# Optimization experiments

Hardware: AMD Instinct MI355X
Metric: run time of the kernel (lower is better)

The kernel has to match this reference:

```python
import jax, jax.numpy as jnp
import numpy as np

N, E, D, L = 100000, 400000, 300, 5
BN_EPS = 1e-5


def setup_inputs() -> dict:
    key = jax.random.key(0)
    ks = jax.random.split(key, 8)
    x = jax.random.randint(ks[0], (N, 7), 0, 5)
    edge_index = jax.random.randint(ks[1], (2, E), 0, N)
    edge_attr = jax.random.randint(ks[2], (E, 4), 0, 2)
    s = 0.1
    atom_tables = jax.random.normal(ks[3], (7, 119, D), jnp.float32) * s
    bond_tables = jax.random.normal(ks[4], (L, 4, 6, D), jnp.float32) * s
    mlp_w1 = jax.random.normal(ks[5], (L, D, 2 * D), jnp.float32) * (1.0 / np.sqrt(D))
    mlp_b1 = jnp.zeros((L, 2 * D), jnp.float32)
    mlp_w2 = jax.random.normal(ks[6], (L, 2 * D, D), jnp.float32) * (1.0 / np.sqrt(2 * D))
    mlp_b2 = jnp.zeros((L, D), jnp.float32)
    bn_gamma = jnp.ones((L, D), jnp.float32)
    bn_beta = jnp.zeros((L, D), jnp.float32)
    return dict(x=x, edge_index=edge_index, edge_attr=edge_attr,
                atom_tables=atom_tables, bond_tables=bond_tables,
                mlp_w1=mlp_w1, mlp_b1=mlp_b1, mlp_w2=mlp_w2, mlp_b2=mlp_b2,
                bn_gamma=bn_gamma, bn_beta=bn_beta)


def reference(x, edge_index, edge_attr, atom_tables, bond_tables,
              mlp_w1, mlp_b1, mlp_w2, mlp_b2, bn_gamma, bn_beta):
    n = x.shape[0]
    # add self loops (PyG add_self_loops appends them)
    loop = jnp.arange(n)
    src = jnp.concatenate([edge_index[0], loop])  # message source j
    dst = jnp.concatenate([edge_index[1], loop])  # aggregation target i
    self_loop_attr = jnp.zeros((n, 4), edge_attr.dtype).at[:, 0].set(4)
    ea = jnp.concatenate([edge_attr, self_loop_attr], axis=0)  # [E+N, 4]

    # AtomEncoder: sum of 7 per-feature embeddings -> [N, D]
    h = atom_tables[jnp.arange(7), x].sum(axis=1)

    for l in range(L):
        # BondEncoder: sum of 4 per-feature embeddings -> [E+N, D]
        e_emb = bond_tables[l][jnp.arange(4), ea].sum(axis=1)
        # GIN message = x_j + edge_emb, aggr='add' by target node
        msg = h[src] + e_emb
        agg = jax.ops.segment_sum(msg, dst, num_segments=n)
        # GIN update MLP: Linear -> ReLU -> Linear
        hid = jax.nn.relu(agg @ mlp_w1[l] + mlp_b1[l])
        out = hid @ mlp_w2[l] + mlp_b2[l]
        # BatchNorm1d (training mode: batch stats, biased var)
        mu = out.mean(axis=0)
        var = out.var(axis=0)
        out = (out - mu) / jnp.sqrt(var + BN_EPS) * bn_gamma[l] + bn_beta[l]
        # drop_ratio = 0.0 -> dropout is identity; ReLU except last layer
        if l < L - 1:
            out = jax.nn.relu(out)
        h = out
    return h  # JK='last'
```

## Files before the change

### kernel.cpp

```cpp
#include <hip/hip_runtime.h>

typedef unsigned short u16;
typedef unsigned int   u32;
typedef __bf16 bf16x8 __attribute__((ext_vector_type(8)));
typedef float  f32x4  __attribute__((ext_vector_type(4)));

__device__ __forceinline__ u16 f2bf(float f) {
    u32 u = __builtin_bit_cast(u32, f);
    u = u + 0x7fffu + ((u >> 16) & 1u);
    return (u16)(u >> 16);
}
__device__ __forceinline__ float bflo(u32 u) { return __builtin_bit_cast(float, u << 16); }
__device__ __forceinline__ float bfhi(u32 u) { return __builtin_bit_cast(float, u & 0xffff0000u); }
__device__ __forceinline__ u32 pack2(float x, float y) { return (u32)f2bf(x) | ((u32)f2bf(y) << 16); }

#define NN 100000
#define EE 400000
#define DP 320
#define HP 640

__global__ void count_deg(const int* __restrict__ ei, int* __restrict__ deg, int E) {
    int e = blockIdx.x * 256 + threadIdx.x;
    if (e < E) atomicAdd(&deg[ei[E + e]], 1);
}

__global__ void scan1(const int* __restrict__ deg, int* __restrict__ out, int* __restrict__ bsums, int n) {
    __shared__ int lds[1024];
    int t = threadIdx.x;
    int i = blockIdx.x * 1024 + t;
    int v = (i < n) ? deg[i] : 0;
    lds[t] = v;
    __syncthreads();
    for (int d = 1; d < 1024; d <<= 1) {
        int add = (t >= d) ? lds[t - d] : 0;
        __syncthreads();
        lds[t] += add;
        __syncthreads();
    }
    if (i < n) out[i] = lds[t] - v;
    if (t == 1023) bsums[blockIdx.x] = lds[t];
}

__global__ void scan2(int* __restrict__ bsums, int nb) {
    __shared__ int lds[128];
    int t = threadIdx.x;
    int v = (t < nb) ? bsums[t] : 0;
    lds[t] = v;
    __syncthreads();
    for (int d = 1; d < 128; d <<= 1) {
        int add = (t >= d) ? lds[t - d] : 0;
        __syncthreads();
        lds[t] += add;
        __syncthreads();
    }
    if (t < nb) bsums[t] = lds[t] - v;
}

__global__ void scan3(int* __restrict__ out, const int* __restrict__ bsums, int n, int etot) {
    int i = blockIdx.x * 1024 + threadIdx.x;
    if (i < n) out[i] += bsums[blockIdx.x];
    else if (i == n) out[i] = etot;
}

__global__ void fill_csr(const int* __restrict__ ei, const int* __restrict__ ea,
                         int* __restrict__ cursors, u32* __restrict__ vals, int E) {
    int e = blockIdx.x * 256 + threadIdx.x;
    if (e >= E) return;
    int dst = ei[E + e];
    int src = ei[e];
    u32 code = (u32)((ea[e*4] & 1) | ((ea[e*4+1] & 1) << 1) | ((ea[e*4+2] & 1) << 2) | ((ea[e*4+3] & 1) << 3));
    int pos = atomicAdd(&cursors[dst], 1);
    vals[pos] = ((u32)src << 4) | code;
}

__global__ void conv_w1(const float* __restrict__ w, u16* __restrict__ wt) {
    int id = blockIdx.x * 256 + threadIdx.x;
    if (id >= 5 * HP * DP) return;
    int l = id / (HP * DP);
    int rem = id - l * (HP * DP);
    int n = rem / DP;
    int k = rem - n * DP;
    u16 v = 0;
    if (n < 600 && k < 300) v = f2bf(w[((size_t)l * 300 + k) * 600 + n]);
    wt[id] = v;
}
__global__ void conv_w2(const float* __restrict__ w, u16* __restrict__ wt) {
    int id = blockIdx.x * 256 + threadIdx.x;
    if (id >= 5 * DP * HP) return;
    int l = id / (DP * HP);
    int rem = id - l * (DP * HP);
    int n = rem / HP;
    int k = rem - n * HP;
    u16 v = 0;
    if (n < 300 && k < 600) v = f2bf(w[((size_t)l * 600 + k) * 300 + n]);
    wt[id] = v;
}

__global__ void atom_enc(const int* __restrict__ x, const float* __restrict__ at, u16* __restrict__ y) {
    const int i = blockIdx.x;
    const int d = threadIdx.x;
    __shared__ int xi[7];
    if (d < 7) xi[d] = x[i * 7 + d];
    __syncthreads();
    u16 v = 0;
    if (d < 300) {
        float s = 0.f;
        #pragma unroll
        for (int f = 0; f < 7; ++f) s += at[(f * 119 + xi[f]) * 300 + d];
        v = f2bf(s);
    }
    y[(size_t)i * DP + d] = v;
}

__global__ void bond_enc(const float* __restrict__ bt, float* __restrict__ emb) {
    const int c = blockIdx.x;
    const int d = threadIdx.x;
    float s = 0.f;
    if (d < 300) {
        if (c < 16) {
            #pragma unroll
            for (int f = 0; f < 4; ++f) s += bt[(f * 6 + ((c >> f) & 1)) * 300 + d];
        } else {
            s = bt[4 * 300 + d];
            #pragma unroll
            for (int f = 1; f < 4; ++f) s += bt[f * 6 * 300 + d];
        }
    }
    emb[c * DP + d] = s;
}

__global__ void bn_ss(const float* __restrict__ stats, const float* __restrict__ gamma,
                      const float* __restrict__ beta, float* __restrict__ scale,
                      float* __restrict__ shift, int n) {
    int d = threadIdx.x;
    float sc = 0.f, sh = 0.f;
    if (d < 300) {
        float inv_n = 1.0f / (float)n;
        float mu = stats[d] * inv_n;
        float var = stats[DP + d] * inv_n - mu * mu;
        float inv = 1.0f / sqrtf(var + 1e-5f);
        sc = gamma[d] * inv;
        sh = beta[d] - mu * sc;
    }
    scale[d] = sc; shift[d] = sh;
}

__global__ void bn_apply(const float* __restrict__ hraw, const float* __restrict__ scale,
                         const float* __restrict__ shift, u16* __restrict__ y) {
    const int i = blockIdx.x;
    const int d = threadIdx.x;
    float v = fmaf(scale[d], hraw[(size_t)i * DP + d], shift[d]);
    y[(size_t)i * DP + d] = f2bf(fmaxf(v, 0.f));
}

__global__ void aggregate(const u16* __restrict__ y,
                          const float* __restrict__ emb,
                          const int* __restrict__ offs, const u32* __restrict__ vals,
                          u16* __restrict__ agg, const int n) {
    const int wid = (int)((blockIdx.x * (size_t)blockDim.x + threadIdx.x) >> 6);
    const int lane = threadIdx.x & 63;
    if (wid >= n) return;
    const int j0 = lane, j1 = lane + 64, j2 = lane + 128;
    const bool has2 = (lane < 32);

    float a0x = 0.f, a0y = 0.f, a1x = 0.f, a1y = 0.f, a2x = 0.f, a2y = 0.f;

    auto accum = [&](int srcrow, const float* erow) {
        const u32* row = (const u32*)y + (size_t)srcrow * (DP / 2);
        u32 u0 = row[j0], u1 = row[j1];
        u32 u2 = has2 ? row[j2] : 0u;
        float2 e0 = *(const float2*)(erow + 2 * j0);
        float2 e1 = *(const float2*)(erow + 2 * j1);
        a0x += bflo(u0) + e0.x;  a0y += bfhi(u0) + e0.y;
        a1x += bflo(u1) + e1.x;  a1y += bfhi(u1) + e1.y;
        if (has2) {
            float2 e2 = *(const float2*)(erow + 2 * j2);
            a2x += bflo(u2) + e2.x;  a2y += bfhi(u2) + e2.y;
        }
    };

    accum(wid, emb + 16 * DP);
    const int s = offs[wid], t = offs[wid + 1];
    for (int e = s; e < t; ++e) {
        u32 v = vals[e];
        accum((int)(v >> 4), emb + (v & 15u) * DP);
    }

    u32* out = (u32*)agg + (size_t)wid * (DP / 2);
    out[j0] = pack2(a0x, a0y);
    out[j1] = pack2(a1x, a1y);
    if (has2) out[j2] = pack2(a2x, a2y);
}

#define ASTR 328
#define HSTR 40

__global__ __launch_bounds__(512, 2) void fused_mlp(
    const u16* __restrict__ A,
    const u16* __restrict__ W1t,
    const u16* __restrict__ W2t,
    const float* __restrict__ b1g,
    const float* __restrict__ b2g,
    float* __restrict__ H,
    float* __restrict__ st1, float* __restrict__ st2,
    const int M) {

    __shared__ __align__(16) u16 As[128 * ASTR];
    __shared__ __align__(16) u16 Wb[2][320 * HSTR];
    __shared__ __align__(16) u16 hidT[128 * HSTR];

    const int tid  = threadIdx.x;
    const int bm   = blockIdx.x * 128;
    const int wave = tid >> 6;
    const int lane = tid & 63;
    const int mg   = wave >> 1;
    const int ng   = wave & 1;
    const int l15  = lane & 15;
    const int q    = lane >> 4;

    #pragma unroll
    for (int it = 0; it < 10; ++it) {
        int u = tid + it * 512;
        int row = u / 40, ku = u - row * 40;
        uint4 v; v.x = v.y = v.z = v.w = 0;
        if (bm + row < M) v = *(const uint4*)(A + (size_t)(bm + row) * DP + ku * 8);
        *(uint4*)&As[row * ASTR + ku * 8] = v;
    }
    {
        uint4 w0 = *(const uint4*)(W1t + (size_t)(tid / 40) * DP + (tid % 40) * 8);
        uint4 w1v = *(const uint4*)(W1t + (size_t)((tid + 512) / 40) * DP + ((tid + 512) % 40) * 8);
        uint4 w2v; w2v.x = w2v.y = w2v.z = w2v.w = 0;
        int u2 = tid + 1024;
        if (u2 < 1280) w2v = *(const uint4*)(W1t + (size_t)(u2 / 40) * DP + (u2 % 40) * 8);
        *(uint4*)&Wb[0][(tid / 40) * ASTR + (tid % 40) * 8] = w0;
        *(uint4*)&Wb[0][((tid + 512) / 40) * ASTR + ((tid + 512) % 40) * 8] = w1v;
        if (u2 < 1280) *(uint4*)&Wb[0][(u2 / 40) * ASTR + (u2 % 40) * 8] = w2v;
    }
    __syncthreads();

    bf16x8 afr[2][10];
    #pragma unroll
    for (int mf = 0; mf < 2; ++mf)
        #pragma unroll
        for (int kt = 0; kt < 10; ++kt) {
            uint4 t = *(const uint4*)&As[(mg * 32 + mf * 16 + l15) * ASTR + kt * 32 + q * 8];
            afr[mf][kt] = __builtin_bit_cast(bf16x8, t);
        }

    f32x4 acc2[2][10];
    const f32x4 zero4 = {0.f, 0.f, 0.f, 0.f};
    #pragma unroll
    for (int mf = 0; mf < 2; ++mf)
        #pragma unroll
        for (int nf = 0; nf < 10; ++nf) acc2[mf][nf] = zero4;

    for (int c = 0; c < 20; ++c) {
        uint4 p0, p1, p2;
        {
            int u0 = tid, u1 = tid + 512, u2 = tid + 1024;
            p0 = *(const uint4*)(W2t + (size_t)(u0 >> 2) * HP + c * 32 + (u0 & 3) * 8);
            p1 = *(const uint4*)(W2t + (size_t)(u1 >> 2) * HP + c * 32 + (u1 & 3) * 8);
            p2.x = p2.y = p2.z = p2.w = 0;
            if (u2 < 1280) p2 = *(const uint4*)(W2t + (size_t)(u2 >> 2) * HP + c * 32 + (u2 & 3) * 8);
        }

        f32x4 acc1[2] = {zero4, zero4};
        #pragma unroll
        for (int kt = 0; kt < 10; ++kt) {
            uint4 t = *(const uint4*)&Wb[0][(ng * 16 + l15) * ASTR + kt * 32 + q * 8];
            bf16x8 bfr = __builtin_bit_cast(bf16x8, t);
            acc1[0] = __builtin_amdgcn_mfma_f32_16x16x32_bf16(afr[0][kt], bfr, acc1[0], 0, 0, 0);
            acc1[1] = __builtin_amdgcn_mfma_f32_16x16x32_bf16(afr[1][kt], bfr, acc1[1], 0, 0, 0);
        }
        {
            int gcol = c * 32 + ng * 16 + l15;
            float bb = (gcol < 600) ? b1g[gcol] : 0.f;
            #pragma unroll
            for (int mf = 0; mf < 2; ++mf)
                #pragma unroll
                for (int r = 0; r < 4; ++r) {
                    float v = fmaxf(acc1[mf][r] + bb, 0.f);
                    hidT[(mg * 32 + mf * 16 + q * 4 + r) * HSTR + ng * 16 + l15] = f2bf(v);
                }
        }
        {
            int u0 = tid, u1 = tid + 512, u2 = tid + 1024;
            *(uint4*)&Wb[1][(u0 >> 2) * HSTR + (u0 & 3) * 8] = p0;
            *(uint4*)&Wb[1][(u1 >> 2) * HSTR + (u1 & 3) * 8] = p1;
            if (u2 < 1280) *(uint4*)&Wb[1][(u2 >> 2) * HSTR + (u2 & 3) * 8] = p2;
        }
        __syncthreads();

        uint4 q0, q1, q2;
        if (c < 19) {
            int u0 = tid, u1 = tid + 512, u2 = tid + 1024;
            const u16* base = W1t + (size_t)(c + 1) * 32 * DP;
            q0 = *(const uint4*)(base + (size_t)(u0 / 40) * DP + (u0 % 40) * 8);
            q1 = *(const uint4*)(base + (size_t)(u1 / 40) * DP + (u1 % 40) * 8);
            q2.x = q2.y = q2.z = q2.w = 0;
            if (u2 < 1280) q2 = *(const uint4*)(base + (size_t)(u2 / 40) * DP + (u2 % 40) * 8);
        }

        bf16x8 a2[2];
        #pragma unroll
        for (int mf = 0; mf < 2; ++mf) {
            uint4 t = *(const uint4*)&hidT[(mg * 32 + mf * 16 + l15) * HSTR + q * 8];
            a2[mf] = __builtin_bit_cast(bf16x8, t);
        }
        #pragma unroll
        for (int nf = 0; nf < 10; ++nf) {
            uint4 t = *(const uint4*)&Wb[1][(ng * 160 + nf * 16 + l15) * HSTR + q * 8];
            bf16x8 bfr = __builtin_bit_cast(bf16x8, t);
            acc2[0][nf] = __builtin_amdgcn_mfma_f32_16x16x32_bf16(a2[0], bfr, acc2[0][nf], 0, 0, 0);
            acc2[1][nf] = __builtin_amdgcn_mfma_f32_16x16x32_bf16(a2[1], bfr, acc2[1][nf], 0, 0, 0);
        }

        if (c < 19) {
            int u0 = tid, u1 = tid + 512, u2 = tid + 1024;
            *(uint4*)&Wb[0][(u0 / 40) * ASTR + (u0 % 40) * 8] = q0;
            *(uint4*)&Wb[0][(u1 / 40) * ASTR + (u1 % 40) * 8] = q1;
            if (u2 < 1280) *(uint4*)&Wb[0][(u2 / 40) * ASTR + (u2 % 40) * 8] = q2;
        }
        __syncthreads();
    }

    #pragma unroll
    for (int nf = 0; nf < 10; ++nf) {
        const int col = ng * 160 + nf * 16 + l15;
        const float bb = (col < 300) ? b2g[col] : 0.f;
        float s1 = 0.f, s2 = 0.f;
        #pragma unroll
        for (int mf = 0; mf < 2; ++mf)
            #pragma unroll
            for (int r = 0; r < 4; ++r) {
                const int row = bm + mg * 32 + mf * 16 + q * 4 + r;
                if (row < M) {
                    float v = acc2[mf][nf][r] + bb;
                    H[(size_t)row * DP + col] = v;
                    s1 += v; s2 += v * v;
                }
            }
        s1 += __shfl_xor(s1, 16); s1 += __shfl_xor(s1, 32);
        s2 += __shfl_xor(s2, 16); s2 += __shfl_xor(s2, 32);
        if (q == 0) { atomicAdd(&st1[col], s1); atomicAdd(&st2[col], s2); }
    }
}

__global__ void finalize(const float* __restrict__ hraw, const float* __restrict__ scale,
                         const float* __restrict__ shift, float* __restrict__ out) {
    const int i = blockIdx.x;
    const int d = threadIdx.x;
    if (d < 300) {
        float x = hraw[(size_t)i * DP + d];
        out[(size_t)i * 300 + d] = fmaf(scale[d], x, shift[d]);
    }
}

extern "C" void kernel_launch(void* const* d_in, const int* in_sizes, int n_in,
                              void* d_out, int out_size, void* d_ws, size_t ws_size,
                              hipStream_t stream) {
    const int N = NN, E = EE, L = 5;
    const int*   x     = (const int*)d_in[0];
    const int*   ei    = (const int*)d_in[1];
    const int*   ea    = (const int*)d_in[2];
    const float* at    = (const float*)d_in[3];
    const float* bt    = (const float*)d_in[4];
    const float* w1    = (const float*)d_in[5];
    const float* b1    = (const float*)d_in[6];
    const float* w2    = (const float*)d_in[7];
    const float* b2    = (const float*)d_in[8];
    const float* gamma = (const float*)d_in[9];
    const float* beta  = (const float*)d_in[10];
    float* out = (float*)d_out;

    char* ws = (char*)d_ws;
    size_t off = 0;
    auto alloc = [&](size_t bytes) { char* p = ws + off; off = (off + bytes + 255) & ~(size_t)255; return p; };
    u16* buf_y    = (u16*)alloc((size_t)N * DP * 2);
    u16* buf_agg  = (u16*)alloc((size_t)N * DP * 2);
    float* buf_h  = (float*)alloc((size_t)N * DP * 4);
    u16* w1t      = (u16*)alloc((size_t)5 * HP * DP * 2);
    u16* w2t      = (u16*)alloc((size_t)5 * DP * HP * 2);
    int* deg      = (int*)alloc((size_t)N * 4);
    int* offs     = (int*)alloc((size_t)(N + 1) * 4);
    int* cursors  = (int*)alloc((size_t)N * 4);
    u32* vals     = (u32*)alloc((size_t)E * 4);
    int* bsums    = (int*)alloc(128 * 4);
    float* emb    = (float*)alloc(17 * DP * 4);
    float* stats  = (float*)alloc(2 * DP * 4);
    float* scale  = (float*)alloc(DP * 4);
    float* shift  = (float*)alloc(DP * 4);

    (void)hipMemsetAsync(deg, 0, (size_t)N * 4, stream);
    count_deg<<<(E + 255) / 256, 256, 0, stream>>>(ei, deg, E);
    const int nb = (N + 1023) / 1024;
    scan1<<<nb, 1024, 0, stream>>>(deg, offs, bsums, N);
    scan2<<<1, 128, 0, stream>>>(bsums, nb);
    scan3<<<(N + 1 + 1023) / 1024, 1024, 0, stream>>>(offs, bsums, N, E);
    (void)hipMemcpyAsync(cursors, offs, (size_t)N * 4, hipMemcpyDeviceToDevice, stream);
    fill_csr<<<(E + 255) / 256, 256, 0, stream>>>(ei, ea, cursors, vals, E);

    conv_w1<<<(5 * HP * DP + 255) / 256, 256, 0, stream>>>(w1, w1t);
    conv_w2<<<(5 * DP * HP + 255) / 256, 256, 0, stream>>>(w2, w2t);

    atom_enc<<<N, DP, 0, stream>>>(x, at, buf_y);

    const int MB = (N + 127) / 128;
    for (int l = 0; l < L; ++l) {
        bond_enc<<<17, DP, 0, stream>>>(bt + (size_t)l * 4 * 6 * 300, emb);
        aggregate<<<(N * 64 + 255) / 256, 256, 0, stream>>>(
            buf_y, emb, offs, vals, buf_agg, N);
        (void)hipMemsetAsync(stats, 0, 2 * DP * 4, stream);
        fused_mlp<<<MB, 512, 0, stream>>>(
            buf_agg,
            w1t + (size_t)l * HP * DP, w2t + (size_t)l * DP * HP,
            b1 + (size_t)l * 600, b2 + (size_t)l * 300,
            buf_h, stats, stats + DP, N);
        bn_ss<<<1, DP, 0, stream>>>(stats, gamma + (size_t)l * 300, beta + (size_t)l * 300, scale, shift, N);
        if (l < L - 1)
            bn_apply<<<N, DP, 0, stream>>>(buf_h, scale, shift, buf_y);
    }
    finalize<<<N, DP, 0, stream>>>(buf_h, scale, shift, out);
}
```

Baseline: 2.150 ms.

## Restructure fused MLP to per-wave tiles with direct global weight loads

The fused MLP kernel drops its shared-memory staging of A and weight tiles. Each wave now owns 16 rows and reads W1/W2 fragments straight from global memory (relying on L2 cache), with 64-row blocks of 256 threads and a small per-wave hidden buffer, so the per-chunk block barriers go away. BatchNorm statistics are first reduced in shared memory before global atomics, which cuts global atomic traffic. The aggregate kernel unrolls the edge loop by four so more gathers are in flight. The risk is extra global and L2 traffic for weights, since each wave reloads the full weight matrices, and higher register pressure from 20 accumulators per wave.

```diff
diff --git a/kernel.cpp b/kernel.cpp
--- a/kernel.cpp
+++ b/kernel.cpp
@@ -165,37 +165,53 @@
 
     float a0x = 0.f, a0y = 0.f, a1x = 0.f, a1y = 0.f, a2x = 0.f, a2y = 0.f;
 
-    auto accum = [&](int srcrow, const float* erow) {
-        const u32* row = (const u32*)y + (size_t)srcrow * (DP / 2);
-        u32 u0 = row[j0], u1 = row[j1];
-        u32 u2 = has2 ? row[j2] : 0u;
-        float2 e0 = *(const float2*)(erow + 2 * j0);
-        float2 e1 = *(const float2*)(erow + 2 * j1);
+    auto addrow = [&](u32 u0, u32 u1, u32 u2, const float* er) {
+        float2 e0 = *(const float2*)(er + 2 * j0);
+        float2 e1 = *(const float2*)(er + 2 * j1);
         a0x += bflo(u0) + e0.x;  a0y += bfhi(u0) + e0.y;
         a1x += bflo(u1) + e1.x;  a1y += bfhi(u1) + e1.y;
         if (has2) {
-            float2 e2 = *(const float2*)(erow + 2 * j2);
+            float2 e2 = *(const float2*)(er + 2 * j2);
             a2x += bflo(u2) + e2.x;  a2y += bfhi(u2) + e2.y;
         }
     };
 
-    accum(wid, emb + 16 * DP);
-    const int s = offs[wid], t = offs[wid + 1];
-    for (int e = s; e < t; ++e) {
+    {
+        const u32* r = (const u32*)y + (size_t)wid * (DP / 2);
+        addrow(r[j0], r[j1], has2 ? r[j2] : 0u, emb + 16 * DP);
+    }
+    int e = offs[wid];
+    const int t = offs[wid + 1];
+    for (; e + 4 <= t; e += 4) {
+        u32 v0 = vals[e], v1 = vals[e + 1], v2 = vals[e + 2], v3 = vals[e + 3];
+        const u32* r0 = (const u32*)y + (size_t)(v0 >> 4) * (DP / 2);
+        const u32* r1 = (const u32*)y + (size_t)(v1 >> 4) * (DP / 2);
+        const u32* r2 = (const u32*)y + (size_t)(v2 >> 4) * (DP / 2);
+        const u32* r3 = (const u32*)y + (size_t)(v3 >> 4) * (DP / 2);
+        u32 x00 = r0[j0], x01 = r0[j1], x02 = has2 ? r0[j2] : 0u;
+        u32 x10 = r1[j0], x11 = r1[j1], x12 = has2 ? r1[j2] : 0u;
+        u32 x20 = r2[j0], x21 = r2[j1], x22 = has2 ? r2[j2] : 0u;
+        u32 x30 = r3[j0], x31 = r3[j1], x32 = has2 ? r3[j2] : 0u;
+        addrow(x00, x01, x02, emb + (v0 & 15u) * DP);
+        addrow(x10, x11, x12, emb + (v1 & 15u) * DP);
+        addrow(x20, x21, x22, emb + (v2 & 15u) * DP);
+        addrow(x30, x31, x32, emb + (v3 & 15u) * DP);
+    }
+    for (; e < t; ++e) {
         u32 v = vals[e];
-        accum((int)(v >> 4), emb + (v & 15u) * DP);
-    }
-
-    u32* out = (u32*)agg + (size_t)wid * (DP / 2);
-    out[j0] = pack2(a0x, a0y);
-    out[j1] = pack2(a1x, a1y);
-    if (has2) out[j2] = pack2(a2x, a2y);
-}
-
-#define ASTR 328
+        const u32* r = (const u32*)y + (size_t)(v >> 4) * (DP / 2);
+        addrow(r[j0], r[j1], has2 ? r[j2] : 0u, emb + (v & 15u) * DP);
+    }
+
+    u32* outp = (u32*)agg + (size_t)wid * (DP / 2);
+    outp[j0] = pack2(a0x, a0y);
+    outp[j1] = pack2(a1x, a1y);
+    if (has2) outp[j2] = pack2(a2x, a2y);
+}
+
 #define HSTR 40
 
-__global__ __launch_bounds__(512, 2) void fused_mlp(
+__global__ __launch_bounds__(256, 3) void fused_mlp(
     const u16* __restrict__ A,
     const u16* __restrict__ W1t,
     const u16* __restrict__ W2t,
@@ -205,144 +221,91 @@
     float* __restrict__ st1, float* __restrict__ st2,
     const int M) {
 
-    __shared__ __align__(16) u16 As[128 * ASTR];
-    __shared__ __align__(16) u16 Wb[2][320 * HSTR];
-    __shared__ __align__(16) u16 hidT[128 * HSTR];
+    __shared__ __align__(16) u16 hid[64 * HSTR];
+    __shared__ float sst[2 * DP];
 
     const int tid  = threadIdx.x;
-    const int bm   = blockIdx.x * 128;
-    const int wave = tid >> 6;
+    const int wid  = tid >> 6;
     const int lane = tid & 63;
-    const int mg   = wave >> 1;
-    const int ng   = wave & 1;
     const int l15  = lane & 15;
     const int q    = lane >> 4;
-
+    const int bm   = blockIdx.x * 64;
+
+    sst[tid] = 0.f; sst[tid + 256] = 0.f;
+    if (tid < 128) sst[tid + 512] = 0.f;
+    __syncthreads();
+
+    const int row_a = bm + wid * 16 + l15;
+    const bool rv = (row_a < M);
+    const u16* arow = A + (size_t)row_a * DP + q * 8;
+    bf16x8 afr[10];
     #pragma unroll
-    for (int it = 0; it < 10; ++it) {
-        int u = tid + it * 512;
-        int row = u / 40, ku = u - row * 40;
-        uint4 v; v.x = v.y = v.z = v.w = 0;
-        if (bm + row < M) v = *(const uint4*)(A + (size_t)(bm + row) * DP + ku * 8);
-        *(uint4*)&As[row * ASTR + ku * 8] = v;
-    }
-    {
-        uint4 w0 = *(const uint4*)(W1t + (size_t)(tid / 40) * DP + (tid % 40) * 8);
-        uint4 w1v = *(const uint4*)(W1t + (size_t)((tid + 512) / 40) * DP + ((tid + 512) % 40) * 8);
-        uint4 w2v; w2v.x = w2v.y = w2v.z = w2v.w = 0;
-        int u2 = tid + 1024;
-        if (u2 < 1280) w2v = *(const uint4*)(W1t + (size_t)(u2 / 40) * DP + (u2 % 40) * 8);
-        *(uint4*)&Wb[0][(tid / 40) * ASTR + (tid % 40) * 8] = w0;
-        *(uint4*)&Wb[0][((tid + 512) / 40) * ASTR + ((tid + 512) % 40) * 8] = w1v;
-        if (u2 < 1280) *(uint4*)&Wb[0][(u2 / 40) * ASTR + (u2 % 40) * 8] = w2v;
-    }
-    __syncthreads();
-
-    bf16x8 afr[2][10];
+    for (int kt = 0; kt < 10; ++kt) {
+        uint4 tv; tv.x = tv.y = tv.z = tv.w = 0;
+        if (rv) tv = *(const uint4*)(arow + kt * 32);
+        afr[kt] = __builtin_bit_cast(bf16x8, tv);
+    }
+
+    f32x4 acc2[20];
     #pragma unroll
-    for (int mf = 0; mf < 2; ++mf)
+    for (int nf = 0; nf < 20; ++nf) acc2[nf] = (f32x4){0.f, 0.f, 0.f, 0.f};
+
+    const u16* w1l = W1t + (size_t)l15 * DP + q * 8;
+    const u16* w2l = W2t + (size_t)l15 * HP + q * 8;
+    u16* hw = &hid[(wid * 16) * HSTR];
+
+    for (int c = 0; c < 20; ++c) {
+        f32x4 acc1[2] = {(f32x4){0.f,0.f,0.f,0.f}, (f32x4){0.f,0.f,0.f,0.f}};
+        const u16* w1c = w1l + (size_t)(c * 32) * DP;
         #pragma unroll
         for (int kt = 0; kt < 10; ++kt) {
-            uint4 t = *(const uint4*)&As[(mg * 32 + mf * 16 + l15) * ASTR + kt * 32 + q * 8];
-            afr[mf][kt] = __builtin_bit_cast(bf16x8, t);
-        }
-
-    f32x4 acc2[2][10];
-    const f32x4 zero4 = {0.f, 0.f, 0.f, 0.f};
-    #pragma unroll
-    for (int mf = 0; mf < 2; ++mf)
-        #pragma unroll
-        for (int nf = 0; nf < 10; ++nf) acc2[mf][nf] = zero4;
-
-    for (int c = 0; c < 20; ++c) {
-        uint4 p0, p1, p2;
-        {
-            int u0 = tid, u1 = tid + 512, u2 = tid + 1024;
-            p0 = *(const uint4*)(W2t + (size_t)(u0 >> 2) * HP + c * 32 + (u0 & 3) * 8);
-            p1 = *(const uint4*)(W2t + (size_t)(u1 >> 2) * HP + c * 32 + (u1 & 3) * 8);
-            p2.x = p2.y = p2.z = p2.w = 0;
-            if (u2 < 1280) p2 = *(const uint4*)(W2t + (size_t)(u2 >> 2) * HP + c * 32 + (u2 & 3) * 8);
-        }
-
-        f32x4 acc1[2] = {zero4, zero4};
-        #pragma unroll
-        for (int kt = 0; kt < 10; ++kt) {
-            uint4 t = *(const uint4*)&Wb[0][(ng * 16 + l15) * ASTR + kt * 32 + q * 8];
-            bf16x8 bfr = __builtin_bit_cast(bf16x8, t);
-            acc1[0] = __builtin_amdgcn_mfma_f32_16x16x32_bf16(afr[0][kt], bfr, acc1[0], 0, 0, 0);
-            acc1[1] = __builtin_amdgcn_mfma_f32_16x16x32_bf16(afr[1][kt], bfr, acc1[1], 0, 0, 0);
-        }
-        {
-            int gcol = c * 32 + ng * 16 + l15;
+            bf16x8 wa = __builtin_bit_cast(bf16x8, *(const uint4*)(w1c + kt * 32));
+            bf16x8 wb = __builtin_bit_cast(bf16x8, *(const uint4*)(w1c + (size_t)16 * DP + kt * 32));
+            acc1[0] = __builtin_amdgcn_mfma_f32_16x16x32_bf16(afr[kt], wa, acc1[0], 0, 0, 0);
+            acc1[1] = __builtin_amdgcn_mfma_f32_16x16x32_bf16(afr[kt], wb, acc1[1], 0, 0, 0);
+        }
+        #pragma unroll
+        for (int h = 0; h < 2; ++h) {
+            int gcol = c * 32 + h * 16 + l15;
             float bb = (gcol < 600) ? b1g[gcol] : 0.f;
             #pragma unroll
-            for (int mf = 0; mf < 2; ++mf)
-                #pragma unroll
-                for (int r = 0; r < 4; ++r) {
-                    float v = fmaxf(acc1[mf][r] + bb, 0.f);
-                    hidT[(mg * 32 + mf * 16 + q * 4 + r) * HSTR + ng * 16 + l15] = f2bf(v);
-                }
-        }
-        {
-            int u0 = tid, u1 = tid + 512, u2 = tid + 1024;
-            *(uint4*)&Wb[1][(u0 >> 2) * HSTR + (u0 & 3) * 8] = p0;
-            *(uint4*)&Wb[1][(u1 >> 2) * HSTR + (u1 & 3) * 8] = p1;
-            if (u2 < 1280) *(uint4*)&Wb[1][(u2 >> 2) * HSTR + (u2 & 3) * 8] = p2;
-        }
-        __syncthreads();
-
-        uint4 q0, q1, q2;
-        if (c < 19) {
-            int u0 = tid, u1 = tid + 512, u2 = tid + 1024;
-            const u16* base = W1t + (size_t)(c + 1) * 32 * DP;
-            q0 = *(const uint4*)(base + (size_t)(u0 / 40) * DP + (u0 % 40) * 8);
-            q1 = *(const uint4*)(base + (size_t)(u1 / 40) * DP + (u1 % 40) * 8);
-            q2.x = q2.y = q2.z = q2.w = 0;
-            if (u2 < 1280) q2 = *(const uint4*)(base + (size_t)(u2 / 40) * DP + (u2 % 40) * 8);
-        }
-
-        bf16x8 a2[2];
-        #pragma unroll
-        for (int mf = 0; mf < 2; ++mf) {
-            uint4 t = *(const uint4*)&hidT[(mg * 32 + mf * 16 + l15) * HSTR + q * 8];
-            a2[mf] = __builtin_bit_cast(bf16x8, t);
-        }
-        #pragma unroll
-        for (int nf = 0; nf < 10; ++nf) {
-            uint4 t = *(const uint4*)&Wb[1][(ng * 160 + nf * 16 + l15) * HSTR + q * 8];
-            bf16x8 bfr = __builtin_bit_cast(bf16x8, t);
-            acc2[0][nf] = __builtin_amdgcn_mfma_f32_16x16x32_bf16(a2[0], bfr, acc2[0][nf], 0, 0, 0);
-            acc2[1][nf] = __builtin_amdgcn_mfma_f32_16x16x32_bf16(a2[1], bfr, acc2[1][nf], 0, 0, 0);
-        }
-
-        if (c < 19) {
-            int u0 = tid, u1 = tid + 512, u2 = tid + 1024;
-            *(uint4*)&Wb[0][(u0 / 40) * ASTR + (u0 % 40) * 8] = q0;
-            *(uint4*)&Wb[0][(u1 / 40) * ASTR + (u1 % 40) * 8] = q1;
-            if (u2 < 1280) *(uint4*)&Wb[0][(u2 / 40) * ASTR + (u2 % 40) * 8] = q2;
-        }
-        __syncthreads();
+            for (int r = 0; r < 4; ++r) {
+                float v = fmaxf(acc1[h][r] + bb, 0.f);
+                hw[(q * 4 + r) * HSTR + h * 16 + l15] = f2bf(v);
+            }
+        }
+        bf16x8 a2 = __builtin_bit_cast(bf16x8, *(const uint4*)&hw[l15 * HSTR + q * 8]);
+        const u16* w2c = w2l + c * 32;
+        #pragma unroll
+        for (int nf = 0; nf < 20; ++nf) {
+            bf16x8 wf = __builtin_bit_cast(bf16x8, *(const uint4*)(w2c + (size_t)(nf * 16) * HP));
+            acc2[nf] = __builtin_amdgcn_mfma_f32_16x16x32_bf16(a2, wf, acc2[nf], 0, 0, 0);
+        }
     }
 
     #pragma unroll
-    for (int nf = 0; nf < 10; ++nf) {
-        const int col = ng * 160 + nf * 16 + l15;
+    for (int nf = 0; nf < 20; ++nf) {
+        const int col = nf * 16 + l15;
         const float bb = (col < 300) ? b2g[col] : 0.f;
         float s1 = 0.f, s2 = 0.f;
         #pragma unroll
-        for (int mf = 0; mf < 2; ++mf)
-            #pragma unroll
-            for (int r = 0; r < 4; ++r) {
-                const int row = bm + mg * 32 + mf * 16 + q * 4 + r;
-                if (row < M) {
-                    float v = acc2[mf][nf][r] + bb;
-                    H[(size_t)row * DP + col] = v;
-                    s1 += v; s2 += v * v;
-                }
+        for (int r = 0; r < 4; ++r) {
+            const int row = bm + wid * 16 + q * 4 + r;
+            if (row < M) {
+                float v = acc2[nf][r] + bb;
+                H[(size_t)row * DP + col] = v;
+                s1 += v; s2 += v * v;
             }
+        }
         s1 += __shfl_xor(s1, 16); s1 += __shfl_xor(s1, 32);
         s2 += __shfl_xor(s2, 16); s2 += __shfl_xor(s2, 32);
-        if (q == 0) { atomicAdd(&st1[col], s1); atomicAdd(&st2[col], s2); }
+        if (q == 0) { atomicAdd(&sst[col], s1); atomicAdd(&sst[DP + col], s2); }
+    }
+    __syncthreads();
+    for (int i = tid; i < 2 * DP; i += 256) {
+        float v = sst[i];
+        if (i < DP) atomicAdd(&st1[i], v);
+        else        atomicAdd(&st2[i - DP], v);
     }
 }
 
@@ -405,13 +368,13 @@
 
     atom_enc<<<N, DP, 0, stream>>>(x, at, buf_y);
 
-    const int MB = (N + 127) / 128;
+    const int MBF = (N + 63) / 64;
     for (int l = 0; l < L; ++l) {
         bond_enc<<<17, DP, 0, stream>>>(bt + (size_t)l * 4 * 6 * 300, emb);
         aggregate<<<(N * 64 + 255) / 256, 256, 0, stream>>>(
             buf_y, emb, offs, vals, buf_agg, N);
         (void)hipMemsetAsync(stats, 0, 2 * DP * 4, stream);
-        fused_mlp<<<MB, 512, 0, stream>>>(
+        fused_mlp<<<MBF, 256, 0, stream>>>(
             buf_agg,
             w1t + (size_t)l * HP * DP, w2t + (size_t)l * DP * HP,
             b1 + (size_t)l * 600, b2 + (size_t)l * 300,
```

Result: slower. 4.614 ms (+114.6%).
